# Performance work log

Measured on AMD Instinct MI355X. Metric: run time of the kernel, lower is better.

Reference implementation:

```python
import jax, jax.numpy as jnp
import numpy as np

TEMP = 0.07
BASE_TEMP = 0.07
EPS = 1e-8


def setup_inputs() -> dict:
    key = jax.random.key(0)
    features = jax.random.normal(key, (4096, 2, 128), dtype=jnp.float32)
    return {"features": features}


def reference(features):
    B, V, D = features.shape  # bsz, n_views, dim
    # torch.cat(torch.unbind(features, dim=1), dim=0): view-major ordering
    cf = jnp.swapaxes(features, 0, 1).reshape(V * B, D)  # [N, D], N = V*B
    # cosine similarity = normalize rows then GEMM (same math as broadcasted CosineSimilarity)
    n = cf / jnp.maximum(jnp.linalg.norm(cf, axis=-1, keepdims=True), EPS)
    logits = jnp.matmul(n, n.T) / TEMP  # [N, N]
    N = V * B
    logits_mask = 1.0 - jnp.eye(N, dtype=logits.dtype)  # zero out self-contrast
    # SimCLR mask: eye(B) tiled over (anchor_count, contrast_count), minus diagonal
    pos_mask = jnp.tile(jnp.eye(B, dtype=logits.dtype), (V, V)) * logits_mask
    exp_logits = jnp.exp(logits) * logits_mask
    log_prob = logits - jnp.log(exp_logits.sum(axis=1, keepdims=True))
    mean_log_prob_pos = (pos_mask * log_prob).sum(axis=1) / pos_mask.sum(axis=1)
    loss = -(TEMP / BASE_TEMP) * mean_log_prob_pos
    return loss.reshape(V, B).mean()
```

## Files before the change

kernel.cpp:

```cpp
#include <hip/hip_runtime.h>
#include <hip/hip_bf16.h>
#include <math.h>


constexpr int   Bsz   = 4096;
constexpr int   Nrows = 8192;
constexpr int   Dd    = 128;
constexpr float TEMPf = 0.07f;
constexpr float EPSN  = 1e-8f;
constexpr float SCALE = 1.4426950408889634f / 0.07f;
constexpr float LN2   = 0.6931471805599453f;

constexpr int CHUNKS     = 32;
constexpr int CHUNK_COLS = Nrows / CHUNKS;
constexpr int TILES      = CHUNK_COLS / 32;
constexpr int ROWS_BLK   = 256;
constexpr int YG         = Nrows / ROWS_BLK;
constexpr int PREPBLKS   = Bsz / 4;

typedef __attribute__((ext_vector_type(8)))  short bf16x8;
typedef __attribute__((ext_vector_type(16))) float floatx16;


constexpr size_t OFF_PART = 0x200000;
constexpr size_t OFF_SPOS = 0x300000;

__device__ __forceinline__ void gld_lds16(const void* g, void* l) {
    __builtin_amdgcn_global_load_lds(
        (const __attribute__((address_space(1))) void*)g,
        (__attribute__((address_space(3))) void*)l, 16, 0, 0);
}

__global__ void prep_k(const float* __restrict__ f,
                       char* __restrict__ nF,
                       float* __restrict__ sposPart,
                       float* __restrict__ out) {
    __shared__ float sred[4];
    int tid  = threadIdx.x;
    int wid  = tid >> 6;
    int lane = tid & 63;
    int b    = blockIdx.x * 4 + wid;
    if (blockIdx.x == 0 && tid == 0) out[0] = 0.f;

    const float* s0 = f + (size_t)(b * 2) * Dd;
    float2 x = *(const float2*)(s0 + lane * 2);
    float2 y = *(const float2*)(s0 + Dd + lane * 2);
    float ss0 = x.x * x.x + x.y * x.y;
    float ss1 = y.x * y.x + y.y * y.y;
    float dt  = x.x * y.x + x.y * y.y;
    #pragma unroll
    for (int off = 32; off; off >>= 1) {
        ss0 += __shfl_xor(ss0, off);
        ss1 += __shfl_xor(ss1, off);
        dt  += __shfl_xor(dt,  off);
    }
    float inv0 = 1.0f / fmaxf(sqrtf(ss0), EPSN);
    float inv1 = 1.0f / fmaxf(sqrtf(ss1), EPSN);

    size_t poff = (size_t)(lane >> 3) * 1024 + ((lane >> 2) & 1) * 512
                + (lane & 3) * 4;

    __hip_bfloat162 h;
    h.x = __float2bfloat16(x.x * inv0);
    h.y = __float2bfloat16(x.y * inv0);
    *(__hip_bfloat162*)(nF + (size_t)(b >> 5) * 8192 + (b & 31) * 16 + poff) = h;
    int r1 = Bsz + b;
    h.x = __float2bfloat16(y.x * inv1);
    h.y = __float2bfloat16(y.y * inv1);
    *(__hip_bfloat162*)(nF + (size_t)(r1 >> 5) * 8192 + (r1 & 31) * 16 + poff) = h;

    if (lane == 0) sred[wid] = dt * inv0 * inv1 / TEMPf;
    __syncthreads();
    if (tid == 0) sposPart[blockIdx.x] = sred[0] + sred[1] + sred[2] + sred[3];
}

__global__ __launch_bounds__(256, 3)
void main_k(const char* __restrict__ nF, float* __restrict__ partial) {
    __shared__ char  bufs[2][8192];
    __shared__ float colred[4][256];
    const int tid  = threadIdx.x;
    const int wid  = tid >> 6;
    const int lane = tid & 63;
    const int lo   = lane & 31;
    const int hi   = lane >> 5;
    const int gy   = blockIdx.y;
    const int rbase = gy * ROWS_BLK + wid * 64;
    const int cbase = blockIdx.x * CHUNK_COLS;
    const int cg0   = cbase >> 5;

    bf16x8 afrag[2][8];
    #pragma unroll
    for (int s = 0; s < 2; s++) {
        const char* ag = nF + (size_t)((rbase + s * 32) >> 5) * 8192 + lane * 16;
        #pragma unroll
        for (int kc = 0; kc < 8; kc++)
            afrag[s][kc] = *(const bf16x8*)(ag + kc * 1024);
    }

    {
        const char* g0 = nF + (size_t)cg0 * 8192;
        int kc = wid * 2;
        gld_lds16(g0 + kc * 1024 + lane * 16,       &bufs[0][kc * 1024]);
        gld_lds16(g0 + (kc + 1) * 1024 + lane * 16, &bufs[0][(kc + 1) * 1024]);
    }

    floatx16 zero = {};

    #pragma unroll 1
    for (int t = 0; t < TILES; t++) {
        __syncthreads();
        if (t + 1 < TILES) {
            const char* gn = nF + (size_t)(cg0 + t + 1) * 8192;
            char* dst = bufs[(t + 1) & 1];
            int kc = wid * 2;
            gld_lds16(gn + kc * 1024 + lane * 16,       dst + kc * 1024);
            gld_lds16(gn + (kc + 1) * 1024 + lane * 16, dst + (kc + 1) * 1024);
        }

        const char* buf = bufs[t & 1];
        floatx16 acc0 = zero, acc1 = zero;
        #pragma unroll
        for (int kc = 0; kc < 8; kc++) {
            bf16x8 bf = *(const bf16x8*)&buf[kc * 1024 + lane * 16];
            acc0 = __builtin_amdgcn_mfma_f32_32x32x16_bf16(afrag[0][kc], bf, acc0, 0, 0, 0);
            acc1 = __builtin_amdgcn_mfma_f32_32x32x16_bf16(afrag[1][kc], bf, acc1, 0, 0, 0);
        }

        const int cb32 = cbase + t * 32;
        float cs = 0.f;
        #pragma unroll
        for (int s = 0; s < 2; s++) {
            const floatx16& acc = s ? acc1 : acc0;
            if (cb32 == rbase + s * 32) {
                #pragma unroll
                for (int r = 0; r < 16; r++) {
                    float e = __builtin_amdgcn_exp2f(acc[r] * SCALE);
                    if (lo == ((r & 3) + 8 * (r >> 2) + 4 * hi)) e = 0.f;
                    cs += e;
                }
            } else {
                #pragma unroll
                for (int r = 0; r < 16; r++)
                    cs += __builtin_amdgcn_exp2f(acc[r] * SCALE);
            }
        }
        cs += __shfl_xor(cs, 32);
        if (hi == 0) colred[wid][t * 32 + lo] = cs;
    }

    __syncthreads();
    float v = colred[0][tid] + colred[1][tid] + colred[2][tid] + colred[3][tid];
    partial[(size_t)gy * Nrows + cbase + tid] = v;
}

__global__ __launch_bounds__(256)
void final_k(const float* __restrict__ partial, const float* __restrict__ sposPart,
             float* __restrict__ out) {
    __shared__ float red[4];
    int tid = threadIdx.x;
    int r = blockIdx.x * 256 + tid;
    float se = 0.f;
    #pragma unroll
    for (int p = 0; p < YG; p++) se += partial[(size_t)p * Nrows + r];
    float acc = __builtin_amdgcn_logf(se) * LN2;
    if (tid < 32) acc -= 2.f * sposPart[blockIdx.x * 32 + tid];
    #pragma unroll
    for (int off = 32; off; off >>= 1) acc += __shfl_xor(acc, off);
    if ((tid & 63) == 0) red[tid >> 6] = acc;
    __syncthreads();
    if (tid == 0)
        atomicAdd(out, (red[0] + red[1] + red[2] + red[3]) / (float)Nrows);
}

extern "C" void kernel_launch(void* const* d_in, const int* in_sizes, int n_in,
                              void* d_out, int out_size, void* d_ws, size_t ws_size,
                              hipStream_t stream) {
    const float* f = (const float*)d_in[0];
    char* ws = (char*)d_ws;
    char* nF        = ws;
    float* partial  = (float*)(ws + OFF_PART);
    float* sposPart = (float*)(ws + OFF_SPOS);

    prep_k<<<PREPBLKS, 256, 0, stream>>>(f, nF, sposPart, (float*)d_out);
    dim3 grid(CHUNKS, YG);
    main_k<<<grid, 256, 0, stream>>>(nF, partial);
    final_k<<<Nrows / 256, 256, 0, stream>>>(partial, sposPart, (float*)d_out);
}
```

Before: 78.32 us.

## Fold exp2 scale into normalized features and double tile size per barrier stage

The normalized features are pre-scaled by sqrt(log2(e)/T), so the GEMM output can go straight into exp2 and the per-element multiply in the epilogue disappears. The main loop also stages two 32-column tiles per synchronization, with each wave issuing four async global-to-LDS loads, which halves the number of barriers. LDS use doubles, which could affect occupancy. Rounding the scaled values to bf16 slightly changes numerics, and the positive-pair term is kept unscaled.

Measured after the change: 78.64 us. About the same (+0.4%).

```diff
diff --git a/kernel.cpp b/kernel.cpp
--- a/kernel.cpp
+++ b/kernel.cpp
@@ -14,6 +14,7 @@
 constexpr int CHUNKS     = 32;
 constexpr int CHUNK_COLS = Nrows / CHUNKS;
 constexpr int TILES      = CHUNK_COLS / 32;
+constexpr int STAGES     = TILES / 2;
 constexpr int ROWS_BLK   = 256;
 constexpr int YG         = Nrows / ROWS_BLK;
 constexpr int PREPBLKS   = Bsz / 4;
@@ -42,6 +43,7 @@
     int b    = blockIdx.x * 4 + wid;
     if (blockIdx.x == 0 && tid == 0) out[0] = 0.f;
 
+    const float sqS = sqrtf(SCALE);
     const float* s0 = f + (size_t)(b * 2) * Dd;
     float2 x = *(const float2*)(s0 + lane * 2);
     float2 y = *(const float2*)(s0 + Dd + lane * 2);
@@ -54,8 +56,8 @@
         ss1 += __shfl_xor(ss1, off);
         dt  += __shfl_xor(dt,  off);
     }
-    float inv0 = 1.0f / fmaxf(sqrtf(ss0), EPSN);
-    float inv1 = 1.0f / fmaxf(sqrtf(ss1), EPSN);
+    float inv0 = sqS / fmaxf(sqrtf(ss0), EPSN);
+    float inv1 = sqS / fmaxf(sqrtf(ss1), EPSN);
 
     size_t poff = (size_t)(lane >> 3) * 1024 + ((lane >> 2) & 1) * 512
                 + (lane & 3) * 4;
@@ -69,14 +71,18 @@
     h.y = __float2bfloat16(y.y * inv1);
     *(__hip_bfloat162*)(nF + (size_t)(r1 >> 5) * 8192 + (r1 & 31) * 16 + poff) = h;
 
-    if (lane == 0) sred[wid] = dt * inv0 * inv1 / TEMPf;
+    if (lane == 0) {
+        float i0 = 1.0f / fmaxf(sqrtf(ss0), EPSN);
+        float i1 = 1.0f / fmaxf(sqrtf(ss1), EPSN);
+        sred[wid] = dt * i0 * i1 / TEMPf;
+    }
     __syncthreads();
     if (tid == 0) sposPart[blockIdx.x] = sred[0] + sred[1] + sred[2] + sred[3];
 }
 
 __global__ __launch_bounds__(256, 3)
 void main_k(const char* __restrict__ nF, float* __restrict__ partial) {
-    __shared__ char  bufs[2][8192];
+    __shared__ char  bufs[2][2][8192];
     __shared__ float colred[4][256];
     const int tid  = threadIdx.x;
     const int wid  = tid >> 6;
@@ -98,54 +104,66 @@
     }
 
     {
-        const char* g0 = nF + (size_t)cg0 * 8192;
-        int kc = wid * 2;
-        gld_lds16(g0 + kc * 1024 + lane * 16,       &bufs[0][kc * 1024]);
-        gld_lds16(g0 + (kc + 1) * 1024 + lane * 16, &bufs[0][(kc + 1) * 1024]);
+        const char* gsrc = nF + (size_t)cg0 * 8192;
+        #pragma unroll
+        for (int j = 0; j < 4; j++) {
+            int u = wid * 4 + j;
+            gld_lds16(gsrc + (size_t)u * 1024 + lane * 16,
+                      &bufs[0][u >> 3][(u & 7) * 1024]);
+        }
     }
 
     floatx16 zero = {};
 
     #pragma unroll 1
-    for (int t = 0; t < TILES; t++) {
+    for (int st = 0; st < STAGES; st++) {
         __syncthreads();
-        if (t + 1 < TILES) {
-            const char* gn = nF + (size_t)(cg0 + t + 1) * 8192;
-            char* dst = bufs[(t + 1) & 1];
-            int kc = wid * 2;
-            gld_lds16(gn + kc * 1024 + lane * 16,       dst + kc * 1024);
-            gld_lds16(gn + (kc + 1) * 1024 + lane * 16, dst + (kc + 1) * 1024);
-        }
-
-        const char* buf = bufs[t & 1];
-        floatx16 acc0 = zero, acc1 = zero;
-        #pragma unroll
-        for (int kc = 0; kc < 8; kc++) {
-            bf16x8 bf = *(const bf16x8*)&buf[kc * 1024 + lane * 16];
-            acc0 = __builtin_amdgcn_mfma_f32_32x32x16_bf16(afrag[0][kc], bf, acc0, 0, 0, 0);
-            acc1 = __builtin_amdgcn_mfma_f32_32x32x16_bf16(afrag[1][kc], bf, acc1, 0, 0, 0);
-        }
-
-        const int cb32 = cbase + t * 32;
-        float cs = 0.f;
-        #pragma unroll
-        for (int s = 0; s < 2; s++) {
-            const floatx16& acc = s ? acc1 : acc0;
-            if (cb32 == rbase + s * 32) {
-                #pragma unroll
-                for (int r = 0; r < 16; r++) {
-                    float e = __builtin_amdgcn_exp2f(acc[r] * SCALE);
-                    if (lo == ((r & 3) + 8 * (r >> 2) + 4 * hi)) e = 0.f;
-                    cs += e;
-                }
-            } else {
-                #pragma unroll
-                for (int r = 0; r < 16; r++)
-                    cs += __builtin_amdgcn_exp2f(acc[r] * SCALE);
+        if (st + 1 < STAGES) {
+            const char* gn = nF + (size_t)(cg0 + (st + 1) * 2) * 8192;
+            char* dst0 = bufs[(st + 1) & 1][0];
+            char* dst1 = bufs[(st + 1) & 1][1];
+            #pragma unroll
+            for (int j = 0; j < 4; j++) {
+                int u = wid * 4 + j;
+                gld_lds16(gn + (size_t)u * 1024 + lane * 16,
+                          (u >> 3) ? dst1 + (u & 7) * 1024
+                                   : dst0 + (u & 7) * 1024);
             }
         }
-        cs += __shfl_xor(cs, 32);
-        if (hi == 0) colred[wid][t * 32 + lo] = cs;
+
+        #pragma unroll
+        for (int half = 0; half < 2; half++) {
+            const int t = st * 2 + half;
+            const char* buf = bufs[st & 1][half];
+            floatx16 acc0 = zero, acc1 = zero;
+            #pragma unroll
+            for (int kc = 0; kc < 8; kc++) {
+                bf16x8 bf = *(const bf16x8*)&buf[kc * 1024 + lane * 16];
+                acc0 = __builtin_amdgcn_mfma_f32_32x32x16_bf16(afrag[0][kc], bf, acc0, 0, 0, 0);
+                acc1 = __builtin_amdgcn_mfma_f32_32x32x16_bf16(afrag[1][kc], bf, acc1, 0, 0, 0);
+            }
+
+            const int cb32 = cbase + t * 32;
+            float cs = 0.f;
+            #pragma unroll
+            for (int s = 0; s < 2; s++) {
+                const floatx16& acc = s ? acc1 : acc0;
+                if (cb32 == rbase + s * 32) {
+                    #pragma unroll
+                    for (int r = 0; r < 16; r++) {
+                        float e = __builtin_amdgcn_exp2f(acc[r]);
+                        if (lo == ((r & 3) + 8 * (r >> 2) + 4 * hi)) e = 0.f;
+                        cs += e;
+                    }
+                } else {
+                    #pragma unroll
+                    for (int r = 0; r < 16; r++)
+                        cs += __builtin_amdgcn_exp2f(acc[r]);
+                }
+            }
+            cs += __shfl_xor(cs, 32);
+            if (hi == 0) colred[wid][t * 32 + lo] = cs;
+        }
     }
 
     __syncthreads();
```
